# Kernel optimization log

Measured on AMD Instinct MI355X. Metric: run time of the kernel, lower is better.

Reference implementation:

```python
import jax, jax.numpy as jnp
import numpy as np

N = 100000   # nodes
E = 500000   # edges
D = 128      # h_dim
R = 230      # relation types ('num_edges' in __init__)
B = 64       # num_bases
SI = D // B  # submat_in = 2
SO = D // B  # submat_out = 2
L = 2        # n_hidden_layers
RRELU_SLOPE = (1.0 / 8.0 + 1.0 / 3.0) / 2.0  # F.rrelu eval-mode negative slope


def setup_inputs() -> dict:
    key = jax.random.key(0)
    ks = jax.random.split(key, 9)
    ent_embeds = jax.random.normal(ks[0], (N, D), jnp.float32)
    rel_embeds = jax.random.normal(ks[1], (R, D), jnp.float32)
    # xavier_normal-ish scale for per-relation basis weights and self-loop weights
    weight = jax.random.normal(ks[2], (L, R, B * SI * SO), jnp.float32) * 0.1
    loop_weight = jax.random.normal(ks[3], (L, D, D), jnp.float32) * (2.0 / np.sqrt(2 * D))
    norm = jax.random.uniform(ks[4], (N, 1), jnp.float32)
    node_id = jax.random.randint(ks[5], (N,), 0, N)
    edge_type = jax.random.randint(ks[6], (E,), 0, R)
    src = jax.random.randint(ks[7], (E,), 0, N)
    dst = jax.random.randint(ks[8], (E,), 0, N)
    return dict(ent_embeds=ent_embeds, rel_embeds=rel_embeds, weight=weight,
                loop_weight=loop_weight, norm=norm, node_id=node_id,
                edge_type=edge_type, src=src, dst=dst)


def reference(ent_embeds, rel_embeds, weight, loop_weight, norm,
              node_id, edge_type, src, dst):
    # Aggregator.forward: h = ent_embeds[g.ndata['id']]
    h = ent_embeds[node_id]  # [N, D]
    # (rel_embeds are gathered into g.edata['h'] but unused by RGCNLayer)
    for l in range(L):
        # msg_func: per-edge basis-block weight gather + block-diag bmm
        w = weight[l][edge_type].reshape(E, B, SI, SO)   # [E, B, 2, 2]
        node = h[src].reshape(E, B, SI)                  # [E, B, 2]
        msg = jnp.einsum('ebi,ebio->ebo', node, w).reshape(E, D)
        # update_all scatter-sum + apply_func norm multiply
        agg = jax.ops.segment_sum(msg, dst, num_segments=N) * norm
        # self-loop message (dropout=0)
        agg = agg + h @ loop_weight[l]
        # F.rrelu in eval mode: leaky with slope (lower+upper)/2
        h = jnp.where(agg >= 0, agg, agg * RRELU_SLOPE)
    return h
```

## Files before the change

### kernel.cpp

```cpp
#include <hip/hip_runtime.h>
#include <hip/hip_bf16.h>

#define NN 100000
#define NE 500000
#define DD 128
#define RR 230
#define SLOPE 0.2291666666666666667f

typedef __attribute__((ext_vector_type(8))) short short8;
typedef __attribute__((ext_vector_type(4))) float f32x4;

__device__ __forceinline__ short f2bf(float f) {
    unsigned u = __float_as_uint(f);
    u += 0x7fffu + ((u >> 16) & 1u);
    return (short)(u >> 16);
}
__device__ __forceinline__ float bf2f_lo(unsigned p) { return __uint_as_float(p << 16); }
__device__ __forceinline__ float bf2f_hi(unsigned p) { return __uint_as_float(p & 0xFFFF0000u); }

__global__ __launch_bounds__(256) void hprep_k(const float* __restrict__ ent,
                                               const int* __restrict__ nid,
                                               unsigned short* __restrict__ hb) {
    int gid = blockIdx.x * 256 + threadIdx.x;
    if (gid >= NN * 16) return;
    int n = gid >> 4;
    int u = gid & 15;
    const float* srcp = ent + (size_t)nid[n] * DD + u * 8;
    float4 f0 = *(const float4*)srcp;
    float4 f1 = *(const float4*)(srcp + 4);
    short8 v;
    v[0] = f2bf(f0.x); v[1] = f2bf(f0.y); v[2] = f2bf(f0.z); v[3] = f2bf(f0.w);
    v[4] = f2bf(f1.x); v[5] = f2bf(f1.y); v[6] = f2bf(f1.z); v[7] = f2bf(f1.w);
    *(short8*)(hb + (size_t)n * DD + u * 8) = v;
}

__global__ __launch_bounds__(256) void hist_k(const int* __restrict__ dst,
                                              int* __restrict__ cnt) {
    int e = blockIdx.x * 256 + threadIdx.x;
    if (e >= NE) return;
    atomicAdd(&cnt[dst[e]], 1);
}

__global__ __launch_bounds__(256) void scan1_k(const int* __restrict__ cnt,
                                               int* __restrict__ off,
                                               int* __restrict__ bsum) {
    __shared__ int sh[256];
    int i = blockIdx.x * 256 + threadIdx.x;
    int v = (i < NN) ? cnt[i] : 0;
    sh[threadIdx.x] = v;
    __syncthreads();
    for (int d = 1; d < 256; d <<= 1) {
        int t = (threadIdx.x >= d) ? sh[threadIdx.x - d] : 0;
        __syncthreads();
        sh[threadIdx.x] += t;
        __syncthreads();
    }
    if (i < NN) off[i] = sh[threadIdx.x] - v;
    if (threadIdx.x == 255) bsum[blockIdx.x] = sh[255];
}

__global__ __launch_bounds__(512) void scan2_k(int* __restrict__ bsum, int nb) {
    __shared__ int sh[512];
    int v = (threadIdx.x < nb) ? bsum[threadIdx.x] : 0;
    sh[threadIdx.x] = v;
    __syncthreads();
    for (int d = 1; d < 512; d <<= 1) {
        int t = (threadIdx.x >= d) ? sh[threadIdx.x - d] : 0;
        __syncthreads();
        sh[threadIdx.x] += t;
        __syncthreads();
    }
    if (threadIdx.x < nb) bsum[threadIdx.x] = sh[threadIdx.x] - v;
}

__global__ __launch_bounds__(256) void scan3_k(int* __restrict__ off,
                                               const int* __restrict__ bsum,
                                               int* __restrict__ cursor) {
    int i = blockIdx.x * 256 + threadIdx.x;
    if (i < NN) {
        int o = off[i] + bsum[blockIdx.x];
        off[i] = o;
        cursor[i] = o;
    }
    if (i == 0) off[NN] = NE;
}

__global__ __launch_bounds__(256) void scat_k(const int* __restrict__ src,
                                              const int* __restrict__ et,
                                              const int* __restrict__ dst,
                                              int* __restrict__ cursor,
                                              int* __restrict__ epack) {
    int e = blockIdx.x * 256 + threadIdx.x;
    if (e >= NE) return;
    int pos = atomicAdd(&cursor[dst[e]], 1);
    epack[pos] = (src[e] << 8) | et[e];
}

__global__ __launch_bounds__(256) void wprep_k(const float* __restrict__ lw,
                                               short* __restrict__ wt) {
    int gid = blockIdx.x * 256 + threadIdx.x;
    if (gid >= 2 * DD * 16) return;
    int l   = gid >> 11;
    int rem = gid & 2047;
    int c   = rem >> 4;
    int u   = rem & 15;
    const float* wsrc = lw + l * DD * DD + c;
    short8 v;
    #pragma unroll
    for (int j = 0; j < 8; ++j) v[j] = f2bf(wsrc[(u * 8 + j) * DD]);
    *(short8*)(wt + (size_t)l * DD * DD + c * DD + ((u ^ (c & 7)) << 3)) = v;
}

__global__ __launch_bounds__(256) void agg_k(const unsigned short* __restrict__ hb,
                                             const int* __restrict__ off,
                                             const int* __restrict__ epack,
                                             const float* __restrict__ wl,
                                             const float* __restrict__ norm,
                                             float* __restrict__ agg) {
    int n    = (blockIdx.x * 256 + threadIdx.x) >> 6;
    int lane = threadIdx.x & 63;
    int hl   = lane & 31;
    int h2   = lane >> 5;
    if (n >= NN) return;
    int e0 = off[n];
    int m  = off[n + 1] - e0;
    float a0 = 0.f, a1 = 0.f, a2 = 0.f, a3 = 0.f;

    for (int base = 0; base < m; base += 64) {
        int cnt = m - base;
        if (cnt > 64) cnt = 64;
        int pv = epack[e0 + base + ((lane < cnt) ? lane : cnt - 1)];

        for (int j = 0; j < cnt; j += 8) {
            int i0 = j + 0 + h2, i1 = j + 2 + h2, i2 = j + 4 + h2, i3 = j + 6 + h2;
            int p0 = __shfl(pv, (i0 < cnt) ? i0 : cnt - 1);
            int p1 = __shfl(pv, (i1 < cnt) ? i1 : cnt - 1);
            int p2 = __shfl(pv, (i2 < cnt) ? i2 : cnt - 1);
            int p3 = __shfl(pv, (i3 < cnt) ? i3 : cnt - 1);
            float s0 = (i0 < cnt) ? 1.f : 0.f;
            float s1 = (i1 < cnt) ? 1.f : 0.f;
            float s2 = (i2 < cnt) ? 1.f : 0.f;
            float s3 = (i3 < cnt) ? 1.f : 0.f;
            uint2 xr0 = *(const uint2*)(hb + (size_t)(p0 >> 8) * DD + hl * 4);
            uint2 xr1 = *(const uint2*)(hb + (size_t)(p1 >> 8) * DD + hl * 4);
            uint2 xr2 = *(const uint2*)(hb + (size_t)(p2 >> 8) * DD + hl * 4);
            uint2 xr3 = *(const uint2*)(hb + (size_t)(p3 >> 8) * DD + hl * 4);
            const float* q0 = wl + (size_t)(p0 & 255) * 256 + hl * 8;
            const float* q1 = wl + (size_t)(p1 & 255) * 256 + hl * 8;
            const float* q2 = wl + (size_t)(p2 & 255) * 256 + hl * 8;
            const float* q3 = wl + (size_t)(p3 & 255) * 256 + hl * 8;
            float4 wa0 = *(const float4*)q0, wb0 = *(const float4*)(q0 + 4);
            float4 wa1 = *(const float4*)q1, wb1 = *(const float4*)(q1 + 4);
            float4 wa2 = *(const float4*)q2, wb2 = *(const float4*)(q2 + 4);
            float4 wa3 = *(const float4*)q3, wb3 = *(const float4*)(q3 + 4);
            float4 x0 = make_float4(bf2f_lo(xr0.x) * s0, bf2f_hi(xr0.x) * s0,
                                    bf2f_lo(xr0.y) * s0, bf2f_hi(xr0.y) * s0);
            float4 x1 = make_float4(bf2f_lo(xr1.x) * s1, bf2f_hi(xr1.x) * s1,
                                    bf2f_lo(xr1.y) * s1, bf2f_hi(xr1.y) * s1);
            float4 x2 = make_float4(bf2f_lo(xr2.x) * s2, bf2f_hi(xr2.x) * s2,
                                    bf2f_lo(xr2.y) * s2, bf2f_hi(xr2.y) * s2);
            float4 x3 = make_float4(bf2f_lo(xr3.x) * s3, bf2f_hi(xr3.x) * s3,
                                    bf2f_lo(xr3.y) * s3, bf2f_hi(xr3.y) * s3);
            a0 = fmaf(x0.x, wa0.x, fmaf(x0.y, wa0.z, a0));
            a1 = fmaf(x0.x, wa0.y, fmaf(x0.y, wa0.w, a1));
            a2 = fmaf(x0.z, wb0.x, fmaf(x0.w, wb0.z, a2));
            a3 = fmaf(x0.z, wb0.y, fmaf(x0.w, wb0.w, a3));
            a0 = fmaf(x1.x, wa1.x, fmaf(x1.y, wa1.z, a0));
            a1 = fmaf(x1.x, wa1.y, fmaf(x1.y, wa1.w, a1));
            a2 = fmaf(x1.z, wb1.x, fmaf(x1.w, wb1.z, a2));
            a3 = fmaf(x1.z, wb1.y, fmaf(x1.w, wb1.w, a3));
            a0 = fmaf(x2.x, wa2.x, fmaf(x2.y, wa2.z, a0));
            a1 = fmaf(x2.x, wa2.y, fmaf(x2.y, wa2.w, a1));
            a2 = fmaf(x2.z, wb2.x, fmaf(x2.w, wb2.z, a2));
            a3 = fmaf(x2.z, wb2.y, fmaf(x2.w, wb2.w, a3));
            a0 = fmaf(x3.x, wa3.x, fmaf(x3.y, wa3.z, a0));
            a1 = fmaf(x3.x, wa3.y, fmaf(x3.y, wa3.w, a1));
            a2 = fmaf(x3.z, wb3.x, fmaf(x3.w, wb3.z, a2));
            a3 = fmaf(x3.z, wb3.y, fmaf(x3.w, wb3.w, a3));
        }
    }
    a0 += __shfl_xor(a0, 32);
    a1 += __shfl_xor(a1, 32);
    a2 += __shfl_xor(a2, 32);
    a3 += __shfl_xor(a3, 32);
    if (h2 == 0) {
        float nv = norm[n];
        *(float4*)(agg + (size_t)n * DD + hl * 4) =
            make_float4(a0 * nv, a1 * nv, a2 * nv, a3 * nv);
    }
}

template<int WRITE_BF16>
__global__ __launch_bounds__(256, 2) void apply_k(const float* __restrict__ agg,
                                                  const unsigned short* __restrict__ hb,
                                                  const short* __restrict__ Wt,
                                                  float* __restrict__ outf,
                                                  unsigned short* __restrict__ outb) {
    __shared__ short Ash[DD * DD];
    __shared__ short Wsh[DD * DD];

    const int tid = threadIdx.x;
    const long n0 = (long)blockIdx.x * 128;

    {
        const float4* wsrc = (const float4*)Wt;
        float4*       wdst = (float4*)Wsh;
        #pragma unroll
        for (int i = 0; i < 8; ++i) wdst[tid + i * 256] = wsrc[tid + i * 256];
    }
    {
        const int r  = tid >> 1;
        const int hf = tid & 1;
        long srow = n0 + r;
        if (srow >= NN) srow = NN - 1;
        const unsigned short* hrow = hb + (size_t)srow * DD + hf * 64;
        short* arow = Ash + r * DD;
        #pragma unroll
        for (int uu = 0; uu < 8; ++uu) {
            int u = hf * 8 + uu;
            short8 v = *(const short8*)(hrow + uu * 8);
            *(short8*)(arow + ((u ^ (r & 7)) << 3)) = v;
        }
    }
    __syncthreads();

    const int wv  = tid >> 6;
    const int wm  = wv >> 1;
    const int wn  = wv & 1;
    const int l16 = tid & 15;
    const int q   = (tid & 63) >> 4;

    f32x4 acc[4][4];
    #pragma unroll
    for (int mt = 0; mt < 4; ++mt)
        #pragma unroll
        for (int nt = 0; nt < 4; ++nt) acc[mt][nt] = (f32x4){0.f, 0.f, 0.f, 0.f};

    union Frag { uint2 u2[2]; short8 s8; };

    #pragma unroll
    for (int ks = 0; ks < 4; ++ks) {
        const int ua   = ks * 4 + (q >> 1);
        const int off8 = 4 * (q & 1);
        short8 af[4], bf[4];
        #pragma unroll
        for (int mt = 0; mt < 4; ++mt) {
            int r = wm * 64 + mt * 16 + l16;
            const short* base = Ash + r * DD;
            Frag fr;
            fr.u2[0] = *(const uint2*)(base + ((ua       ^ (r & 7)) << 3) + off8);
            fr.u2[1] = *(const uint2*)(base + (((ua + 2) ^ (r & 7)) << 3) + off8);
            af[mt] = fr.s8;
        }
        #pragma unroll
        for (int nt = 0; nt < 4; ++nt) {
            int c = wn * 64 + nt * 16 + l16;
            const short* base = Wsh + c * DD;
            Frag fr;
            fr.u2[0] = *(const uint2*)(base + ((ua       ^ (c & 7)) << 3) + off8);
            fr.u2[1] = *(const uint2*)(base + (((ua + 2) ^ (c & 7)) << 3) + off8);
            bf[nt] = fr.s8;
        }
        #pragma unroll
        for (int mt = 0; mt < 4; ++mt)
            #pragma unroll
            for (int nt = 0; nt < 4; ++nt)
                acc[mt][nt] = __builtin_amdgcn_mfma_f32_16x16x32_bf16(
                                  af[mt], bf[nt], acc[mt][nt], 0, 0, 0);
    }

    #pragma unroll
    for (int mt = 0; mt < 4; ++mt) {
        #pragma unroll
        for (int i = 0; i < 4; ++i) {
            long nrow = n0 + wm * 64 + mt * 16 + 4 * q + i;
            if (nrow < NN) {
                #pragma unroll
                for (int nt = 0; nt < 4; ++nt) {
                    int c = wn * 64 + nt * 16 + l16;
                    float v = agg[nrow * DD + c] + acc[mt][nt][i];
                    v = (v >= 0.f) ? v : v * SLOPE;
                    if (WRITE_BF16) outb[nrow * DD + c] = (unsigned short)f2bf(v);
                    else            outf[nrow * DD + c] = v;
                }
            }
        }
    }
}

extern "C" void kernel_launch(void* const* d_in, const int* in_sizes, int n_in,
                              void* d_out, int out_size, void* d_ws, size_t ws_size,
                              hipStream_t stream) {
    const float* ent_embeds  = (const float*)d_in[0];
    const float* weight      = (const float*)d_in[2];
    const float* loop_weight = (const float*)d_in[3];
    const float* norm        = (const float*)d_in[4];
    const int*   node_id     = (const int*)d_in[5];
    const int*   edge_type   = (const int*)d_in[6];
    const int*   src         = (const int*)d_in[7];
    const int*   dst         = (const int*)d_in[8];
    float*       out         = (float*)d_out;

    float*          aggbuf = (float*)d_ws;
    unsigned short* hb     = (unsigned short*)(aggbuf + (size_t)NN * DD);
    int*   cnt    = (int*)(hb + (size_t)NN * DD);
    int*   off    = cnt + NN;
    int*   cursor = off + NN + 1;
    int*   bsum   = cursor + NN;
    int*   epack  = bsum + 512;
    short* wt     = (short*)(epack + NE);

    const int NB_E = (NE + 255) / 256;
    const int NB_N = (NN + 255) / 256;

    hipMemsetAsync(cnt, 0, (size_t)NN * sizeof(int), stream);
    wprep_k<<<16,   256, 0, stream>>>(loop_weight, wt);
    hprep_k<<<(NN * 16 + 255) / 256, 256, 0, stream>>>(ent_embeds, node_id, hb);
    hist_k <<<NB_E, 256, 0, stream>>>(dst, cnt);
    scan1_k<<<NB_N, 256, 0, stream>>>(cnt, off, bsum);
    scan2_k<<<1,    512, 0, stream>>>(bsum, NB_N);
    scan3_k<<<NB_N, 256, 0, stream>>>(off, bsum, cursor);
    scat_k <<<NB_E, 256, 0, stream>>>(src, edge_type, dst, cursor, epack);

    const int AGG_BLOCKS = (NN * 64) / 256;
    const int APL_BLOCKS = (NN + 127) / 128;

    agg_k     <<<AGG_BLOCKS, 256, 0, stream>>>(hb, off, epack, weight, norm, aggbuf);
    apply_k<1><<<APL_BLOCKS, 256, 0, stream>>>(aggbuf, hb, wt, nullptr, hb);

    agg_k     <<<AGG_BLOCKS, 256, 0, stream>>>(hb, off, epack,
                                               weight + (size_t)RR * 256, norm, aggbuf);
    apply_k<0><<<APL_BLOCKS, 256, 0, stream>>>(aggbuf, hb, wt + (size_t)DD * DD, out, nullptr);
}
```

Measured before the change: 236.5 us.

## Use bf16 relation weights with dot2 and bf16 aggregation buffer

```diff
diff --git a/kernel.cpp b/kernel.cpp
--- a/kernel.cpp
+++ b/kernel.cpp
@@ -15,22 +15,41 @@
     u += 0x7fffu + ((u >> 16) & 1u);
     return (short)(u >> 16);
 }
-__device__ __forceinline__ float bf2f_lo(unsigned p) { return __uint_as_float(p << 16); }
-__device__ __forceinline__ float bf2f_hi(unsigned p) { return __uint_as_float(p & 0xFFFF0000u); }
+__device__ __forceinline__ unsigned pkbf(float lo, float hi) {
+    return (unsigned)(unsigned short)f2bf(lo) | ((unsigned)(unsigned short)f2bf(hi) << 16);
+}
+
+#if defined(__has_builtin)
+#if __has_builtin(__builtin_amdgcn_fdot2_f32_bf16)
+#define HAS_DOT2 1
+#endif
+#endif
+__device__ __forceinline__ void dot2acc(float& acc, unsigned x, unsigned w) {
+#ifdef HAS_DOT2
+    typedef __attribute__((ext_vector_type(2))) __bf16 bf16x2;
+    acc = __builtin_amdgcn_fdot2_f32_bf16(__builtin_bit_cast(bf16x2, x),
+                                          __builtin_bit_cast(bf16x2, w), acc, false);
+#else
+    acc = fmaf(__uint_as_float(x << 16),        __uint_as_float(w << 16),
+          fmaf(__uint_as_float(x & 0xFFFF0000u), __uint_as_float(w & 0xFFFF0000u), acc));
+#endif
+}
 
 __global__ __launch_bounds__(256) void hprep_k(const float* __restrict__ ent,
                                                const int* __restrict__ nid,
                                                unsigned short* __restrict__ hb) {
     int gid = blockIdx.x * 256 + threadIdx.x;
-    if (gid >= NN * 16) return;
+    if (gid >= (NN + 1) * 16) return;
     int n = gid >> 4;
     int u = gid & 15;
-    const float* srcp = ent + (size_t)nid[n] * DD + u * 8;
-    float4 f0 = *(const float4*)srcp;
-    float4 f1 = *(const float4*)(srcp + 4);
-    short8 v;
-    v[0] = f2bf(f0.x); v[1] = f2bf(f0.y); v[2] = f2bf(f0.z); v[3] = f2bf(f0.w);
-    v[4] = f2bf(f1.x); v[5] = f2bf(f1.y); v[6] = f2bf(f1.z); v[7] = f2bf(f1.w);
+    short8 v = {0, 0, 0, 0, 0, 0, 0, 0};
+    if (n < NN) {
+        const float* srcp = ent + (size_t)nid[n] * DD + u * 8;
+        float4 f0 = *(const float4*)srcp;
+        float4 f1 = *(const float4*)(srcp + 4);
+        v[0] = f2bf(f0.x); v[1] = f2bf(f0.y); v[2] = f2bf(f0.z); v[3] = f2bf(f0.w);
+        v[4] = f2bf(f1.x); v[5] = f2bf(f1.y); v[6] = f2bf(f1.z); v[7] = f2bf(f1.w);
+    }
     *(short8*)(hb + (size_t)n * DD + u * 8) = v;
 }
 
@@ -96,6 +115,23 @@
     epack[pos] = (src[e] << 8) | et[e];
 }
 
+__global__ __launch_bounds__(256) void wbprep_k(const float* __restrict__ weight,
+                                                unsigned* __restrict__ wb) {
+    int gid = blockIdx.x * 256 + threadIdx.x;
+    if (gid >= 2 * RR * 32) return;
+    int lt = gid >> 5;
+    int hl = gid & 31;
+    const float* wsrc = weight + (size_t)lt * 256 + hl * 8;
+    float4 f0 = *(const float4*)wsrc;
+    float4 f1 = *(const float4*)(wsrc + 4);
+    uint4 v;
+    v.x = pkbf(f0.x, f0.z);
+    v.y = pkbf(f0.y, f0.w);
+    v.z = pkbf(f1.x, f1.z);
+    v.w = pkbf(f1.y, f1.w);
+    *(uint4*)(wb + (size_t)lt * 128 + hl * 4) = v;
+}
+
 __global__ __launch_bounds__(256) void wprep_k(const float* __restrict__ lw,
                                                short* __restrict__ wt) {
     int gid = blockIdx.x * 256 + threadIdx.x;
@@ -111,12 +147,13 @@
     *(short8*)(wt + (size_t)l * DD * DD + c * DD + ((u ^ (c & 7)) << 3)) = v;
 }
 
+#define ZP (NN << 8)
 __global__ __launch_bounds__(256) void agg_k(const unsigned short* __restrict__ hb,
                                              const int* __restrict__ off,
                                              const int* __restrict__ epack,
-                                             const float* __restrict__ wl,
+                                             const unsigned* __restrict__ wb,
                                              const float* __restrict__ norm,
-                                             float* __restrict__ agg) {
+                                             unsigned short* __restrict__ aggb) {
     int n    = (blockIdx.x * 256 + threadIdx.x) >> 6;
     int lane = threadIdx.x & 63;
     int hl   = lane & 31;
@@ -125,58 +162,38 @@
     int e0 = off[n];
     int m  = off[n + 1] - e0;
     float a0 = 0.f, a1 = 0.f, a2 = 0.f, a3 = 0.f;
+    const char* hbb = (const char*)hb;
+    const char* wbb = (const char*)wb;
+    const int hoff = hl * 8;
+    const int woff = hl * 16;
 
     for (int base = 0; base < m; base += 64) {
         int cnt = m - base;
         if (cnt > 64) cnt = 64;
-        int pv = epack[e0 + base + ((lane < cnt) ? lane : cnt - 1)];
+        int pv = epack[e0 + base + ((lane < cnt) ? lane : 0)];
 
         for (int j = 0; j < cnt; j += 8) {
-            int i0 = j + 0 + h2, i1 = j + 2 + h2, i2 = j + 4 + h2, i3 = j + 6 + h2;
-            int p0 = __shfl(pv, (i0 < cnt) ? i0 : cnt - 1);
-            int p1 = __shfl(pv, (i1 < cnt) ? i1 : cnt - 1);
-            int p2 = __shfl(pv, (i2 < cnt) ? i2 : cnt - 1);
-            int p3 = __shfl(pv, (i3 < cnt) ? i3 : cnt - 1);
-            float s0 = (i0 < cnt) ? 1.f : 0.f;
-            float s1 = (i1 < cnt) ? 1.f : 0.f;
-            float s2 = (i2 < cnt) ? 1.f : 0.f;
-            float s3 = (i3 < cnt) ? 1.f : 0.f;
-            uint2 xr0 = *(const uint2*)(hb + (size_t)(p0 >> 8) * DD + hl * 4);
-            uint2 xr1 = *(const uint2*)(hb + (size_t)(p1 >> 8) * DD + hl * 4);
-            uint2 xr2 = *(const uint2*)(hb + (size_t)(p2 >> 8) * DD + hl * 4);
-            uint2 xr3 = *(const uint2*)(hb + (size_t)(p3 >> 8) * DD + hl * 4);
-            const float* q0 = wl + (size_t)(p0 & 255) * 256 + hl * 8;
-            const float* q1 = wl + (size_t)(p1 & 255) * 256 + hl * 8;
-            const float* q2 = wl + (size_t)(p2 & 255) * 256 + hl * 8;
-            const float* q3 = wl + (size_t)(p3 & 255) * 256 + hl * 8;
-            float4 wa0 = *(const float4*)q0, wb0 = *(const float4*)(q0 + 4);
-            float4 wa1 = *(const float4*)q1, wb1 = *(const float4*)(q1 + 4);
-            float4 wa2 = *(const float4*)q2, wb2 = *(const float4*)(q2 + 4);
-            float4 wa3 = *(const float4*)q3, wb3 = *(const float4*)(q3 + 4);
-            float4 x0 = make_float4(bf2f_lo(xr0.x) * s0, bf2f_hi(xr0.x) * s0,
-                                    bf2f_lo(xr0.y) * s0, bf2f_hi(xr0.y) * s0);
-            float4 x1 = make_float4(bf2f_lo(xr1.x) * s1, bf2f_hi(xr1.x) * s1,
-                                    bf2f_lo(xr1.y) * s1, bf2f_hi(xr1.y) * s1);
-            float4 x2 = make_float4(bf2f_lo(xr2.x) * s2, bf2f_hi(xr2.x) * s2,
-                                    bf2f_lo(xr2.y) * s2, bf2f_hi(xr2.y) * s2);
-            float4 x3 = make_float4(bf2f_lo(xr3.x) * s3, bf2f_hi(xr3.x) * s3,
-                                    bf2f_lo(xr3.y) * s3, bf2f_hi(xr3.y) * s3);
-            a0 = fmaf(x0.x, wa0.x, fmaf(x0.y, wa0.z, a0));
-            a1 = fmaf(x0.x, wa0.y, fmaf(x0.y, wa0.w, a1));
-            a2 = fmaf(x0.z, wb0.x, fmaf(x0.w, wb0.z, a2));
-            a3 = fmaf(x0.z, wb0.y, fmaf(x0.w, wb0.w, a3));
-            a0 = fmaf(x1.x, wa1.x, fmaf(x1.y, wa1.z, a0));
-            a1 = fmaf(x1.x, wa1.y, fmaf(x1.y, wa1.w, a1));
-            a2 = fmaf(x1.z, wb1.x, fmaf(x1.w, wb1.z, a2));
-            a3 = fmaf(x1.z, wb1.y, fmaf(x1.w, wb1.w, a3));
-            a0 = fmaf(x2.x, wa2.x, fmaf(x2.y, wa2.z, a0));
-            a1 = fmaf(x2.x, wa2.y, fmaf(x2.y, wa2.w, a1));
-            a2 = fmaf(x2.z, wb2.x, fmaf(x2.w, wb2.z, a2));
-            a3 = fmaf(x2.z, wb2.y, fmaf(x2.w, wb2.w, a3));
-            a0 = fmaf(x3.x, wa3.x, fmaf(x3.y, wa3.z, a0));
-            a1 = fmaf(x3.x, wa3.y, fmaf(x3.y, wa3.w, a1));
-            a2 = fmaf(x3.z, wb3.x, fmaf(x3.w, wb3.z, a2));
-            a3 = fmaf(x3.z, wb3.y, fmaf(x3.w, wb3.w, a3));
+            int i0 = j + h2, i1 = j + 2 + h2, i2 = j + 4 + h2, i3 = j + 6 + h2;
+            int p0 = (i0 < cnt) ? __shfl(pv, i0) : ZP;
+            int p1 = (i1 < cnt) ? __shfl(pv, i1) : ZP;
+            int p2 = (i2 < cnt) ? __shfl(pv, i2) : ZP;
+            int p3 = (i3 < cnt) ? __shfl(pv, i3) : ZP;
+            uint2 x0 = *(const uint2*)(hbb + (p0 & 0xFFFFFF00u) + hoff);
+            uint2 x1 = *(const uint2*)(hbb + (p1 & 0xFFFFFF00u) + hoff);
+            uint2 x2 = *(const uint2*)(hbb + (p2 & 0xFFFFFF00u) + hoff);
+            uint2 x3 = *(const uint2*)(hbb + (p3 & 0xFFFFFF00u) + hoff);
+            uint4 w0 = *(const uint4*)(wbb + ((p0 & 255) << 9) + woff);
+            uint4 w1 = *(const uint4*)(wbb + ((p1 & 255) << 9) + woff);
+            uint4 w2 = *(const uint4*)(wbb + ((p2 & 255) << 9) + woff);
+            uint4 w3 = *(const uint4*)(wbb + ((p3 & 255) << 9) + woff);
+            dot2acc(a0, x0.x, w0.x); dot2acc(a1, x0.x, w0.y);
+            dot2acc(a2, x0.y, w0.z); dot2acc(a3, x0.y, w0.w);
+            dot2acc(a0, x1.x, w1.x); dot2acc(a1, x1.x, w1.y);
+            dot2acc(a2, x1.y, w1.z); dot2acc(a3, x1.y, w1.w);
+            dot2acc(a0, x2.x, w2.x); dot2acc(a1, x2.x, w2.y);
+            dot2acc(a2, x2.y, w2.z); dot2acc(a3, x2.y, w2.w);
+            dot2acc(a0, x3.x, w3.x); dot2acc(a1, x3.x, w3.y);
+            dot2acc(a2, x3.y, w3.z); dot2acc(a3, x3.y, w3.w);
         }
     }
     a0 += __shfl_xor(a0, 32);
@@ -185,13 +202,15 @@
     a3 += __shfl_xor(a3, 32);
     if (h2 == 0) {
         float nv = norm[n];
-        *(float4*)(agg + (size_t)n * DD + hl * 4) =
-            make_float4(a0 * nv, a1 * nv, a2 * nv, a3 * nv);
+        uint2 pk;
+        pk.x = pkbf(a0 * nv, a1 * nv);
+        pk.y = pkbf(a2 * nv, a3 * nv);
+        *(uint2*)(aggb + (size_t)n * DD + hl * 4) = pk;
     }
 }
 
 template<int WRITE_BF16>
-__global__ __launch_bounds__(256, 2) void apply_k(const float* __restrict__ agg,
+__global__ __launch_bounds__(256, 2) void apply_k(const unsigned short* __restrict__ aggb,
                                                   const unsigned short* __restrict__ hb,
                                                   const short* __restrict__ Wt,
                                                   float* __restrict__ outf,
@@ -278,7 +297,8 @@
                 #pragma unroll
                 for (int nt = 0; nt < 4; ++nt) {
                     int c = wn * 64 + nt * 16 + l16;
-                    float v = agg[nrow * DD + c] + acc[mt][nt][i];
+                    float g = __uint_as_float((unsigned)aggb[nrow * DD + c] << 16);
+                    float v = g + acc[mt][nt][i];
                     v = (v >= 0.f) ? v : v * SLOPE;
                     if (WRITE_BF16) outb[nrow * DD + c] = (unsigned short)f2bf(v);
                     else            outf[nrow * DD + c] = v;
@@ -301,34 +321,36 @@
     const int*   dst         = (const int*)d_in[8];
     float*       out         = (float*)d_out;
 
-    float*          aggbuf = (float*)d_ws;
-    unsigned short* hb     = (unsigned short*)(aggbuf + (size_t)NN * DD);
-    int*   cnt    = (int*)(hb + (size_t)NN * DD);
+    unsigned short* aggb = (unsigned short*)d_ws;
+    unsigned short* hb   = aggb + (size_t)NN * DD;
+    int*   cnt    = (int*)(hb + (size_t)(NN + 1) * DD);
     int*   off    = cnt + NN;
     int*   cursor = off + NN + 1;
     int*   bsum   = cursor + NN;
     int*   epack  = bsum + 512;
     short* wt     = (short*)(epack + NE);
+    unsigned* wb  = (unsigned*)(wt + 2 * DD * DD);
 
     const int NB_E = (NE + 255) / 256;
     const int NB_N = (NN + 255) / 256;
 
     hipMemsetAsync(cnt, 0, (size_t)NN * sizeof(int), stream);
-    wprep_k<<<16,   256, 0, stream>>>(loop_weight, wt);
-    hprep_k<<<(NN * 16 + 255) / 256, 256, 0, stream>>>(ent_embeds, node_id, hb);
-    hist_k <<<NB_E, 256, 0, stream>>>(dst, cnt);
-    scan1_k<<<NB_N, 256, 0, stream>>>(cnt, off, bsum);
-    scan2_k<<<1,    512, 0, stream>>>(bsum, NB_N);
-    scan3_k<<<NB_N, 256, 0, stream>>>(off, bsum, cursor);
-    scat_k <<<NB_E, 256, 0, stream>>>(src, edge_type, dst, cursor, epack);
+    wprep_k <<<16, 256, 0, stream>>>(loop_weight, wt);
+    wbprep_k<<<(2 * RR * 32 + 255) / 256, 256, 0, stream>>>(weight, wb);
+    hprep_k <<<((NN + 1) * 16 + 255) / 256, 256, 0, stream>>>(ent_embeds, node_id, hb);
+    hist_k  <<<NB_E, 256, 0, stream>>>(dst, cnt);
+    scan1_k <<<NB_N, 256, 0, stream>>>(cnt, off, bsum);
+    scan2_k <<<1,    512, 0, stream>>>(bsum, NB_N);
+    scan3_k <<<NB_N, 256, 0, stream>>>(off, bsum, cursor);
+    scat_k  <<<NB_E, 256, 0, stream>>>(src, edge_type, dst, cursor, epack);
 
     const int AGG_BLOCKS = (NN * 64) / 256;
     const int APL_BLOCKS = (NN + 127) / 128;
 
-    agg_k     <<<AGG_BLOCKS, 256, 0, stream>>>(hb, off, epack, weight, norm, aggbuf);
-    apply_k<1><<<APL_BLOCKS, 256, 0, stream>>>(aggbuf, hb, wt, nullptr, hb);
-
-    agg_k     <<<AGG_BLOCKS, 256, 0, stream>>>(hb, off, epack,
-                                               weight + (size_t)RR * 256, norm, aggbuf);
-    apply_k<0><<<APL_BLOCKS, 256, 0, stream>>>(aggbuf, hb, wt + (size_t)DD * DD, out, nullptr);
-}
+    agg_k     <<<AGG_BLOCKS, 256, 0, stream>>>(hb, off, epack, wb, norm, aggb);
+    apply_k<1><<<APL_BLOCKS, 256, 0, stream>>>(aggb, hb, wt, nullptr, hb);
+
+    agg_k     <<<AGG_BLOCKS, 256, 0, stream>>>(hb, off, epack, wb + (size_t)RR * 128,
+                                               norm, aggb);
+    apply_k<0><<<APL_BLOCKS, 256, 0, stream>>>(aggb, hb, wt + (size_t)DD * DD, out, nullptr);
+}
```

Result: faster. 212.5 us (-10.1%).
